# Kernel tuning notes

Hardware: AMD Instinct MI355X
Metric: run time of the kernel (lower is better)

The kernel has to match this reference:

```python
import jax, jax.numpy as jnp
import numpy as np


def setup_inputs() -> dict:
    key = jax.random.key(0)
    ks = jax.random.split(key, 7)
    B, T, H, FUT = 512, 512, 256, 1
    s = 1.0 / np.sqrt(H)
    return {
        "ts": jax.random.normal(ks[0], (B, T), dtype=jnp.float32),
        "W_ih": jax.random.normal(ks[1], (4 * H, 1), dtype=jnp.float32) * s,
        "W_hh": jax.random.normal(ks[2], (4 * H, H), dtype=jnp.float32) * s,
        "b_ih": jax.random.normal(ks[3], (4 * H,), dtype=jnp.float32) * s,
        "b_hh": jax.random.normal(ks[4], (4 * H,), dtype=jnp.float32) * s,
        "W_out": jax.random.normal(ks[5], (FUT, T * H), dtype=jnp.float32) * (1.0 / np.sqrt(T * H)),
        "b_out": jax.random.normal(ks[6], (FUT,), dtype=jnp.float32) * 0.01,
    }


def _lstm(ts, W_ih, W_hh, b_ih, b_hh):
    # ts: [B, T] scalar series -> input_size = 1
    B, T = ts.shape
    H = W_hh.shape[1]
    # Precompute input contribution for all timesteps: [B, T, 4H]
    xg = ts[:, :, None] * W_ih[:, 0][None, None, :] + (b_ih + b_hh)
    xg = jnp.transpose(xg, (1, 0, 2))  # [T, B, 4H]

    def step(carry, xg_t):
        h, c = carry
        gates = xg_t + h @ W_hh.T  # [B, 4H]
        i, f, g, o = jnp.split(gates, 4, axis=-1)  # PyTorch gate order i,f,g,o
        c_new = jax.nn.sigmoid(f) * c + jax.nn.sigmoid(i) * jnp.tanh(g)
        h_new = jax.nn.sigmoid(o) * jnp.tanh(c_new)
        return (h_new, c_new), h_new

    h0 = jnp.zeros((B, H), dtype=ts.dtype)
    c0 = jnp.zeros((B, H), dtype=ts.dtype)
    _, hs = jax.lax.scan(step, (h0, c0), xg)  # hs: [T, B, H]
    return jnp.transpose(hs, (1, 0, 2))  # [B, T, H]


def reference(ts, W_ih, W_hh, b_ih, b_hh, W_out, b_out):
    B, T = ts.shape
    lstm_out = _lstm(ts, W_ih, W_hh, b_ih, b_hh)  # [B, T, H]
    flat = lstm_out.reshape(B, -1)  # [B, T*H]
    return flat @ W_out.T + b_out  # [B, future]
```

## Files before the change

### kernel.cpp

```cpp
#include <hip/hip_runtime.h>


typedef _Float16 half8 __attribute__((ext_vector_type(8)));
typedef float f32x4 __attribute__((ext_vector_type(4)));
typedef float f32x2 __attribute__((ext_vector_type(2)));

constexpr int kT = 512;
constexpr int kHF = 264;
constexpr float kLog2e = 1.44269504088896340736f;

#define ATL(p)    __hip_atomic_load((p), __ATOMIC_RELAXED, __HIP_MEMORY_SCOPE_AGENT)
#define ATS(p, v) __hip_atomic_store((p), (v), __ATOMIC_RELAXED, __HIP_MEMORY_SCOPE_AGENT)

__global__ void prep_weights(const float* __restrict__ W_hh, _Float16* __restrict__ ws)
{
    int gid = blockIdx.x * blockDim.x + threadIdx.x;
    int lane = gid & 63;
    int f = (gid >> 6) & 127;
    int sub = gid >> 13;
    int kt = f & 7, g = (f >> 3) & 3, c = f >> 5;
    int R = g * 256 + sub * 64 + c * 16 + (lane & 15);
    int k = kt * 32 + (lane >> 4) * 8;
    float s = (g == 2) ? 2.0f * kLog2e : -kLog2e;
    const float* src = W_hh + R * 256 + k;
    half8 v;
    #pragma unroll
    for (int j = 0; j < 8; ++j) v[j] = (_Float16)(src[j] * s);
    reinterpret_cast<half8*>(ws)[gid] = v;
}

__device__ __forceinline__ f32x4 mfma16(half8 a, half8 b, f32x4 c) {
    return __builtin_amdgcn_mfma_f32_16x16x32_f16(a, b, c, 0, 0, 0);
}

__global__ __launch_bounds__(512, 2)
void lstm_main(const float* __restrict__ ts,
               const float* __restrict__ W_ih,
               const float* __restrict__ b_ih,
               const float* __restrict__ b_hh,
               const float* __restrict__ W_out,
               const _Float16* __restrict__ wfrag,
               unsigned long long* __restrict__ gb64,
               float* __restrict__ pbuf)
{
    __shared__ __align__(16) _Float16 wlds[32768];
    __shared__ __align__(16) _Float16 h_full[16][kHF];
    __shared__ __align__(16) float pacc1[4][2][4][16][10];
    __shared__ float red[4][8];

    const int tid  = threadIdx.x;
    const int w    = tid >> 6;
    const int lane = tid & 63;
    const int l16  = lane & 15;
    const int quad = lane >> 4;
    const int bid  = blockIdx.x;
    const int sub  = bid & 3;
    const int grp  = bid >> 2;
    const int b0   = grp * 8;
    const int c    = w & 3;
    const int kh   = w >> 2;

    const half8* wf8 = reinterpret_cast<const half8*>(wfrag) + sub * 8192;
    half8* wl8 = reinterpret_cast<half8*>(wlds);

    for (int i = tid; i < 4096; i += 512) {
        int f = i >> 6, ln = i & 63;
        int jj = f & 1, kh_ = (f >> 1) & 1, g_ = (f >> 2) & 3, c_ = f >> 4;
        wl8[i] = wf8[(((c_ * 4 + g_) * 8) + kh_ * 4 + 2 + jj) * 64 + ln];
    }
    for (int i = tid; i < 16 * kHF; i += 512) (&h_full[0][0])[i] = (_Float16)0.0f;

    unsigned int wr_[8][4];
    #pragma unroll
    for (int g = 0; g < 4; ++g)
        #pragma unroll
        for (int jj = 0; jj < 2; ++jj) {
            uint4 v = *reinterpret_cast<const uint4*>(
                &wf8[(((c * 4 + g) * 8) + kh * 4 + jj) * 64 + lane]);
            int i = g * 2 + jj;
            wr_[i][0] = v.x; wr_[i][1] = v.y; wr_[i][2] = v.z; wr_[i][3] = v.w;
            asm volatile("" : "+v"(wr_[i][0]), "+v"(wr_[i][1]), "+v"(wr_[i][2]), "+v"(wr_[i][3]));
        }

    float wih[4], bias[4];
    #pragma unroll
    for (int g = 0; g < 4; ++g) {
        int R = g * 256 + sub * 64 + c * 16 + l16;
        float s = (g == 2) ? 2.0f * kLog2e : -kLog2e;
        wih[g]  = W_ih[R] * s;
        bias[g] = (b_ih[R] + b_hh[R]) * s;
    }

    const int cs    = tid >> 7;
    const int psub  = (sub + cs) & 3;
    const int pbid  = (grp << 2) | psub;
    const int i0    = tid & 127;
    const int chl   = i0 >> 1;
    const int cm0   = (i0 & 1) * 4;
    unsigned long long* myt[2] = { gb64 + (bid * 2 + 0) * 256, gb64 + (bid * 2 + 1) * 256 };

    float cst[2]  = {0.f, 0.f};
    float oacc[2] = {0.f, 0.f};

    __syncthreads();

    for (int t = 0; t < kT; ++t) {
        const int wpar = t & 1, rp = (t + 1) & 1;

        #pragma unroll
        for (int i = 0; i < 8; ++i)
            asm volatile("" : "+v"(wr_[i][0]), "+v"(wr_[i][1]), "+v"(wr_[i][2]), "+v"(wr_[i][3]));

        float tsv[2] = {0.f, 0.f};
        float wo = 0.f;
        if (quad < 2) {
            #pragma unroll
            for (int rr = 0; rr < 2; ++rr)
                tsv[rr] = ts[(b0 + quad * 4 + kh * 2 + rr) * kT + t];
            wo = W_out[t * 256 + sub * 64 + c * 16 + l16];
        }

        if (cs >= 1) {
            const unsigned long long* pt = gb64 + (pbid * 2 + rp) * 256 + i0 * 2;
            unsigned long long v0, v1;
            const unsigned long long want = (unsigned long long)t;
            for (;;) {
                v0 = ATL(pt);
                v1 = ATL(pt + 1);
                if ((v0 >> 32) == want && (v1 >> 32) == want) break;
                __builtin_amdgcn_s_sleep(1);
            }
            union { unsigned int u; unsigned short s[2]; } a0, a1;
            a0.u = (unsigned int)v0; a1.u = (unsigned int)v1;
            reinterpret_cast<unsigned short*>(&h_full[cm0 + 0][psub * 64 + chl])[0] = a0.s[0];
            reinterpret_cast<unsigned short*>(&h_full[cm0 + 1][psub * 64 + chl])[0] = a0.s[1];
            reinterpret_cast<unsigned short*>(&h_full[cm0 + 2][psub * 64 + chl])[0] = a1.s[0];
            reinterpret_cast<unsigned short*>(&h_full[cm0 + 3][psub * 64 + chl])[0] = a1.s[1];
        }
        __syncthreads();

        half8 a[4];
        #pragma unroll
        for (int j = 0; j < 4; ++j)
            a[j] = *reinterpret_cast<const half8*>(&h_full[l16][(kh * 4 + j) * 32 + quad * 8]);
        f32x4 gacc[4];
        #pragma unroll
        for (int g = 0; g < 4; ++g) { f32x4 z = {0.f, 0.f, 0.f, 0.f}; gacc[g] = z; }
        #pragma unroll
        for (int jj = 0; jj < 2; ++jj)
            #pragma unroll
            for (int g = 0; g < 4; ++g) {
                int i = g * 2 + jj;
                half8 wv = __builtin_bit_cast(half8,
                    make_uint4(wr_[i][0], wr_[i][1], wr_[i][2], wr_[i][3]));
                gacc[g] = mfma16(a[jj], wv, gacc[g]);
            }
        #pragma unroll
        for (int jj = 0; jj < 2; ++jj)
            #pragma unroll
            for (int g = 0; g < 4; ++g)
                gacc[g] = mfma16(a[2 + jj],
                                 wl8[(((c * 4 + g) * 4) + kh * 2 + jj) * 64 + lane], gacc[g]);

        #pragma unroll
        for (int g = 0; g < 4; ++g) {
            f32x2 v; v.x = gacc[g][(1 - kh) * 2 + 0]; v.y = gacc[g][(1 - kh) * 2 + 1];
            *reinterpret_cast<f32x2*>(&pacc1[c][kh][g][l16][quad * 2]) = v;
        }
        __syncthreads();

        if (quad < 2) {
            f32x2 p[4];
            #pragma unroll
            for (int g = 0; g < 4; ++g)
                p[g] = *reinterpret_cast<const f32x2*>(&pacc1[c][1 - kh][g][l16][quad * 2]);
            const int hl = c * 16 + l16;
            const int hk = sub * 64 + hl;
            union { unsigned int u; unsigned short s[2]; } hp;
            #pragma unroll
            for (int rr = 0; rr < 2; ++rr) {
                int ro = kh * 2 + rr;
                float pg[4] = { rr ? p[0].y : p[0].x, rr ? p[1].y : p[1].x,
                                rr ? p[2].y : p[2].x, rr ? p[3].y : p[3].x };
                float gi = gacc[0][ro] + pg[0] + (tsv[rr] * wih[0] + bias[0]);
                float gf = gacc[1][ro] + pg[1] + (tsv[rr] * wih[1] + bias[1]);
                float gg = gacc[2][ro] + pg[2] + (tsv[rr] * wih[2] + bias[2]);
                float go = gacc[3][ro] + pg[3] + (tsv[rr] * wih[3] + bias[3]);
                float I = __builtin_amdgcn_rcpf(1.0f + __builtin_amdgcn_exp2f(gi));
                float F = __builtin_amdgcn_rcpf(1.0f + __builtin_amdgcn_exp2f(gf));
                float G = 1.0f - 2.0f * __builtin_amdgcn_rcpf(1.0f + __builtin_amdgcn_exp2f(gg));
                float O = __builtin_amdgcn_rcpf(1.0f + __builtin_amdgcn_exp2f(go));
                float cn = F * cst[rr] + I * G;
                cst[rr] = cn;
                float tc = 1.0f - 2.0f * __builtin_amdgcn_rcpf(
                               1.0f + __builtin_amdgcn_exp2f(2.0f * kLog2e * cn));
                float hv = O * tc;
                oacc[rr] += hv * wo;
                _Float16 h16 = (_Float16)hv;
                hp.s[rr] = __builtin_bit_cast(unsigned short, h16);
                h_full[quad * 4 + ro][hk] = h16;
            }
            unsigned long long rec = ((unsigned long long)(t + 1) << 32) | hp.u;
            ATS(myt[wpar] + (hl * 4 + quad * 2 + kh), rec);
        }
    }

    #pragma unroll
    for (int rr = 0; rr < 2; ++rr) {
        float v = oacc[rr];
        v += __shfl_xor(v, 1, 64);
        v += __shfl_xor(v, 2, 64);
        v += __shfl_xor(v, 4, 64);
        v += __shfl_xor(v, 8, 64);
        if (l16 == 0 && quad < 2) red[c][quad * 4 + kh * 2 + rr] = v;
    }
    __syncthreads();
    if (tid < 8) {
        float s = 0.f;
        #pragma unroll
        for (int cc = 0; cc < 4; ++cc) s += red[cc][tid];
        pbuf[bid * 8 + tid] = s;
    }
}

__global__ void finalize(const float* __restrict__ pbuf,
                         const float* __restrict__ b_out,
                         float* __restrict__ out)
{
    int b = blockIdx.x * blockDim.x + threadIdx.x;
    int grp = b >> 3, m = b & 7;
    float s = b_out[0];
    #pragma unroll
    for (int s4 = 0; s4 < 4; ++s4) s += pbuf[((grp * 4 + s4) * 8) + m];
    out[b] = s;
}

extern "C" void kernel_launch(void* const* d_in, const int* in_sizes, int n_in,
                              void* d_out, int out_size, void* d_ws, size_t ws_size,
                              hipStream_t stream) {
    const float* ts    = (const float*)d_in[0];
    const float* W_ih  = (const float*)d_in[1];
    const float* W_hh  = (const float*)d_in[2];
    const float* b_ih  = (const float*)d_in[3];
    const float* b_hh  = (const float*)d_in[4];
    const float* W_out = (const float*)d_in[5];
    const float* b_out = (const float*)d_in[6];

    char* wsb = (char*)d_ws;
    _Float16*           wfrag = (_Float16*)wsb;
    unsigned long long* gb64  = (unsigned long long*)(wsb + 524288);
    float*              pbuf  = (float*)(wsb + 1572864);

    hipMemsetAsync(wsb + 524288, 0, 1048576 + 8192, stream);
    prep_weights<<<128, 256, 0, stream>>>(W_hh, wfrag);
    lstm_main<<<256, 512, 0, stream>>>(ts, W_ih, b_ih, b_hh, W_out,
                                       wfrag, gb64, pbuf);
    finalize<<<1, 512, 0, stream>>>(pbuf, b_out, (float*)d_out);
}
```

Before: 995.7 us.

## Add fast non-atomic dwordx4 polling path and remap blocks so partner blocks share an XCD

Each block now also writes its h records to a second buffer with plain global stores, and consumers poll that buffer with a single sc0 dwordx4 load for a bounded number of spins. If the spin limit runs out, the consumer permanently falls back to the original atomic 64-bit polling. The block-to-(group, sub) mapping is changed so the four sub-blocks of a group are spread by stride 8, which likely places them on the same XCD and shares L2, cutting cross-die exchange latency. The cost is an extra store per record and double the sync buffer, and the fast path depends on non-atomic visibility and cache behaviour.

Result: slower. 1.590 ms (+59.7%).

```diff
diff --git a/kernel.cpp b/kernel.cpp
--- a/kernel.cpp
+++ b/kernel.cpp
@@ -4,9 +4,11 @@
 typedef _Float16 half8 __attribute__((ext_vector_type(8)));
 typedef float f32x4 __attribute__((ext_vector_type(4)));
 typedef float f32x2 __attribute__((ext_vector_type(2)));
+typedef unsigned int u32x4 __attribute__((ext_vector_type(4)));
 
 constexpr int kT = 512;
 constexpr int kHF = 264;
+constexpr int kFastSpin = 256;
 constexpr float kLog2e = 1.44269504088896340736f;
 
 #define ATL(p)    __hip_atomic_load((p), __ATOMIC_RELAXED, __HIP_MEMORY_SCOPE_AGENT)
@@ -41,6 +43,7 @@
                const float* __restrict__ W_out,
                const _Float16* __restrict__ wfrag,
                unsigned long long* __restrict__ gb64,
+               unsigned long long* __restrict__ fgb,
                float* __restrict__ pbuf)
 {
     __shared__ __align__(16) _Float16 wlds[32768];
@@ -54,8 +57,8 @@
     const int l16  = lane & 15;
     const int quad = lane >> 4;
     const int bid  = blockIdx.x;
-    const int sub  = bid & 3;
-    const int grp  = bid >> 2;
+    const int sub  = (bid >> 3) & 3;
+    const int grp  = ((bid & 7) << 3) | (bid >> 5);
     const int b0   = grp * 8;
     const int c    = w & 3;
     const int kh   = w >> 2;
@@ -93,14 +96,16 @@
 
     const int cs    = tid >> 7;
     const int psub  = (sub + cs) & 3;
-    const int pbid  = (grp << 2) | psub;
+    const int pbid  = (bid & ~24) | (psub << 3);
     const int i0    = tid & 127;
     const int chl   = i0 >> 1;
     const int cm0   = (i0 & 1) * 4;
-    unsigned long long* myt[2] = { gb64 + (bid * 2 + 0) * 256, gb64 + (bid * 2 + 1) * 256 };
+    unsigned long long* myt[2]  = { gb64 + (bid * 2 + 0) * 256, gb64 + (bid * 2 + 1) * 256 };
+    unsigned long long* fmyt[2] = { fgb  + (bid * 2 + 0) * 256, fgb  + (bid * 2 + 1) * 256 };
 
     float cst[2]  = {0.f, 0.f};
     float oacc[2] = {0.f, 0.f};
+    int fastok = 1;
 
     __syncthreads();
 
@@ -121,17 +126,35 @@
         }
 
         if (cs >= 1) {
-            const unsigned long long* pt = gb64 + (pbid * 2 + rp) * 256 + i0 * 2;
-            unsigned long long v0, v1;
-            const unsigned long long want = (unsigned long long)t;
-            for (;;) {
-                v0 = ATL(pt);
-                v1 = ATL(pt + 1);
-                if ((v0 >> 32) == want && (v1 >> 32) == want) break;
-                __builtin_amdgcn_s_sleep(1);
-            }
+            const int roff = (pbid * 2 + rp) * 256 + i0 * 2;
             union { unsigned int u; unsigned short s[2]; } a0, a1;
-            a0.u = (unsigned int)v0; a1.u = (unsigned int)v1;
+            int got = 0;
+            if (fastok) {
+                const unsigned long long* ptf = fgb + roff;
+                const unsigned int want = (unsigned int)t;
+                u32x4 vv;
+                for (int sp = 0; sp < kFastSpin; ++sp) {
+                    asm volatile("global_load_dwordx4 %0, %1, off sc0\n\t"
+                                 "s_waitcnt vmcnt(0)"
+                                 : "=&v"(vv) : "v"(ptf) : "memory");
+                    if (vv.y == want && vv.w == want) { got = 1; break; }
+                    __builtin_amdgcn_s_sleep(1);
+                }
+                if (got) { a0.u = vv.x; a1.u = vv.z; }
+                else fastok = 0;
+            }
+            if (!got) {
+                const unsigned long long* pt = gb64 + roff;
+                const unsigned long long want = (unsigned long long)t;
+                unsigned long long v0, v1;
+                for (;;) {
+                    v0 = ATL(pt);
+                    v1 = ATL(pt + 1);
+                    if ((v0 >> 32) == want && (v1 >> 32) == want) break;
+                    __builtin_amdgcn_s_sleep(1);
+                }
+                a0.u = (unsigned int)v0; a1.u = (unsigned int)v1;
+            }
             reinterpret_cast<unsigned short*>(&h_full[cm0 + 0][psub * 64 + chl])[0] = a0.s[0];
             reinterpret_cast<unsigned short*>(&h_full[cm0 + 1][psub * 64 + chl])[0] = a0.s[1];
             reinterpret_cast<unsigned short*>(&h_full[cm0 + 2][psub * 64 + chl])[0] = a1.s[0];
@@ -201,7 +224,11 @@
                 h_full[quad * 4 + ro][hk] = h16;
             }
             unsigned long long rec = ((unsigned long long)(t + 1) << 32) | hp.u;
-            ATS(myt[wpar] + (hl * 4 + quad * 2 + kh), rec);
+            const int ridx = hl * 4 + quad * 2 + kh;
+            unsigned long long* fdst = fmyt[wpar] + ridx;
+            asm volatile("global_store_dwordx2 %0, %1, off"
+                         :: "v"(fdst), "v"(rec) : "memory");
+            ATS(myt[wpar] + ridx, rec);
         }
     }
 
@@ -219,7 +246,7 @@
         float s = 0.f;
         #pragma unroll
         for (int cc = 0; cc < 4; ++cc) s += red[cc][tid];
-        pbuf[bid * 8 + tid] = s;
+        pbuf[(grp * 4 + sub) * 8 + tid] = s;
     }
 }
 
@@ -249,11 +276,12 @@
     char* wsb = (char*)d_ws;
     _Float16*           wfrag = (_Float16*)wsb;
     unsigned long long* gb64  = (unsigned long long*)(wsb + 524288);
-    float*              pbuf  = (float*)(wsb + 1572864);
-
-    hipMemsetAsync(wsb + 524288, 0, 1048576 + 8192, stream);
+    unsigned long long* fgb   = (unsigned long long*)(wsb + 1572864);
+    float*              pbuf  = (float*)(wsb + 2621440);
+
+    hipMemsetAsync(wsb + 524288, 0, 2105344, stream);
     prep_weights<<<128, 256, 0, stream>>>(W_hh, wfrag);
     lstm_main<<<256, 512, 0, stream>>>(ts, W_ih, b_ih, b_hh, W_out,
-                                       wfrag, gb64, pbuf);
+                                       wfrag, gb64, fgb, pbuf);
     finalize<<<1, 512, 0, stream>>>(pbuf, b_out, (float*)d_out);
 }
```
